# Kernel optimization log

Hardware: AMD Instinct MI355X
Metric: run time of the kernel (lower is better)

## Reference

```python
import jax, jax.numpy as jnp
import numpy as np

N, F_IN, F_OUT = 8192, 256, 128
ALPHA = 0.2  # LeakyReLU negative slope
NEG_INF = -9e15


def setup_inputs() -> dict:
    key = jax.random.key(0)
    k1, k2, k3, k4 = jax.random.split(key, 4)
    h = jax.random.normal(k1, (N, F_IN), dtype=jnp.float32)
    adj = jax.random.randint(k2, (N, N), 0, 2, dtype=jnp.int32)
    # Xavier-uniform-like init (gain=1.414)
    lim_w = 1.414 * np.sqrt(6.0 / (F_IN + F_OUT))
    W = jax.random.uniform(k3, (F_IN, F_OUT), dtype=jnp.float32, minval=-lim_w, maxval=lim_w)
    lim_a = 1.414 * np.sqrt(6.0 / (2 * F_OUT + 1))
    a = jax.random.uniform(k4, (2 * F_OUT, 1), dtype=jnp.float32, minval=-lim_a, maxval=lim_a)
    return {"h": h, "adj": adj, "W": W, "a": a}


def reference(h, adj, W, a):
    # Wh: [N, F_OUT]
    Wh = h @ W
    f_out = W.shape[1]
    # The torch code builds an [N, N, 2F] concat tensor; mathematically
    # e_ij = leakyrelu(a1 . Wh_i + a2 . Wh_j), so compute via two projections.
    a1 = a[:f_out, 0]   # [F_OUT]
    a2 = a[f_out:, 0]   # [F_OUT]
    f1 = Wh @ a1        # [N]
    f2 = Wh @ a2        # [N]
    e = jax.nn.leaky_relu(f1[:, None] + f2[None, :], negative_slope=ALPHA)  # [N, N]
    e = jnp.where(adj > 0, e, NEG_INF)
    attention = jax.nn.softmax(e, axis=1)  # [N, N]; dropout p=0 (eval mode)
    h_prime = attention @ Wh               # [N, F_OUT]
    return jax.nn.elu(h_prime)
```

## Files before the change

### kernel.cpp

```cpp
#include <hip/hip_runtime.h>
#include <hip/hip_bf16.h>
#include <math.h>

typedef short short8 __attribute__((ext_vector_type(8)));
typedef float f32x4 __attribute__((ext_vector_type(4)));
typedef int i32x4 __attribute__((ext_vector_type(4)));

#define NN 8192
#define FIN 256
#define FOUT 128
#define LRELU_A 0.2f
#define L2E 1.44269504088896f

__device__ __forceinline__ short f2bf(float x) {
    unsigned u = __builtin_bit_cast(unsigned, x);
    unsigned r = (u + 0x7FFFu + ((u >> 16) & 1u)) >> 16;
    return (short)r;
}

__global__ __launch_bounds__(256) void k_pack(const int* __restrict__ adj,
                                              unsigned* __restrict__ packed) {
    __shared__ unsigned char nib[2048];
    const int row = blockIdx.x;
    const int tid = threadIdx.x;
    const i32x4* base = (const i32x4*)(adj + (size_t)row * NN);
    #pragma unroll
    for (int q = 0; q < 8; ++q) {
        int idx = q * 256 + tid;
        i32x4 v = __builtin_nontemporal_load(base + idx);
        unsigned b = (unsigned)(v.x & 1)        | ((unsigned)(v.y & 1) << 1) |
                     ((unsigned)(v.z & 1) << 2) | ((unsigned)(v.w & 1) << 3);
        nib[idx] = (unsigned char)b;
    }
    __syncthreads();
    unsigned long long n8 = *(const unsigned long long*)&nib[tid * 8];
    unsigned w = 0;
    #pragma unroll
    for (int j = 0; j < 8; ++j)
        w |= ((unsigned)((n8 >> (8 * j)) & 0xFull)) << (4 * j);
    packed[(size_t)row * (NN / 32) + tid] = w;
}

__global__ __launch_bounds__(256) void k_wh(const float* __restrict__ h,
                                            const float* __restrict__ W,
                                            const float* __restrict__ a,
                                            float* __restrict__ Wh,
                                            float* __restrict__ f1,
                                            float* __restrict__ f2) {
    __shared__ float hs[8][FIN];
    const int tid = threadIdx.x;
    const int r0 = blockIdx.x * 8;
    #pragma unroll
    for (int i = 0; i < 2; ++i) {
        int f4 = tid + 256 * i;
        int row = f4 >> 6;
        int k4 = (f4 & 63) << 2;
        *(float4*)&hs[row][k4] = *(const float4*)(h + (size_t)(r0 + row) * FIN + k4);
    }
    __syncthreads();
    const int c4 = (tid & 31) * 4;
    const int row = tid >> 5;
    float acc0 = 0.f, acc1 = 0.f, acc2 = 0.f, acc3 = 0.f;
    #pragma unroll 4
    for (int k = 0; k < FIN; ++k) {
        float hv = hs[row][k];
        float4 w4 = *(const float4*)(W + (size_t)k * FOUT + c4);
        acc0 = fmaf(hv, w4.x, acc0);
        acc1 = fmaf(hv, w4.y, acc1);
        acc2 = fmaf(hv, w4.z, acc2);
        acc3 = fmaf(hv, w4.w, acc3);
    }
    float4 o; o.x = acc0; o.y = acc1; o.z = acc2; o.w = acc3;
    *(float4*)(Wh + (size_t)(r0 + row) * FOUT + c4) = o;

    float4 a1v = *(const float4*)(a + c4);
    float4 a2v = *(const float4*)(a + FOUT + c4);
    float p1 = acc0 * a1v.x + acc1 * a1v.y + acc2 * a1v.z + acc3 * a1v.w;
    float p2 = acc0 * a2v.x + acc1 * a2v.y + acc2 * a2v.z + acc3 * a2v.w;
    #pragma unroll
    for (int m = 1; m <= 16; m <<= 1) {
        p1 += __shfl_xor(p1, m, 64);
        p2 += __shfl_xor(p2, m, 64);
    }
    if ((tid & 31) == 0) {
        f1[r0 + row] = p1;
        f2[r0 + row] = p2;
    }
}

__global__ __launch_bounds__(256) void k_transpose(const float* __restrict__ Wh,
                                                   short* __restrict__ WhT) {
    __shared__ float t32[32][33];
    const int tid = threadIdx.x;
    const int tx = tid & 31, ty = tid >> 5;
    const int rb = (blockIdx.x & 255) * 32;
    const int cb = (blockIdx.x >> 8) * 32;
    #pragma unroll
    for (int q = 0; q < 4; ++q) {
        int r = ty + q * 8;
        t32[r][tx] = Wh[(size_t)(rb + r) * FOUT + cb + tx];
    }
    __syncthreads();
    #pragma unroll
    for (int q = 0; q < 4; ++q) {
        int c = ty + q * 8;
        WhT[(size_t)(cb + c) * NN + rb + tx] = f2bf(t32[tx][c]);
    }
}

__global__ __launch_bounds__(256) void k_gmax(const float* __restrict__ f2,
                                              float* __restrict__ gmax) {
    const int tid = threadIdx.x;
    float m = -1e30f;
    for (int i = tid; i < NN; i += 256) m = fmaxf(m, f2[i]);
    #pragma unroll
    for (int s = 1; s <= 32; s <<= 1) m = fmaxf(m, __shfl_xor(m, s, 64));
    __shared__ float red[4];
    if ((tid & 63) == 0) red[tid >> 6] = m;
    __syncthreads();
    if (tid == 0) gmax[0] = fmaxf(fmaxf(red[0], red[1]), fmaxf(red[2], red[3]));
}

__device__ __forceinline__ void gat_body(const short* __restrict__ lrd, unsigned m8,
                                         float4 fa, float4 fb,
                                         float f1r, float mh2, float& den,
                                         f32x4 acc[8]) {
    short8 b0 = *(const short8*)(lrd + 0 * 1024);
    short8 b1 = *(const short8*)(lrd + 1 * 1024);
    short8 b2 = *(const short8*)(lrd + 2 * 1024);
    short8 b3 = *(const short8*)(lrd + 3 * 1024);
    short8 b4 = *(const short8*)(lrd + 4 * 1024);
    short8 b5 = *(const short8*)(lrd + 5 * 1024);
    short8 b6 = *(const short8*)(lrd + 6 * 1024);
    short8 b7 = *(const short8*)(lrd + 7 * 1024);

    float fv[8] = {fa.x, fa.y, fa.z, fa.w, fb.x, fb.y, fb.z, fb.w};
    short8 af;
    #pragma unroll
    for (int i = 0; i < 8; ++i) {
        float e = f1r + fv[i];
        e = fmaxf(e, LRELU_A * e);
        float p = __builtin_amdgcn_exp2f(fmaf(e, L2E, -mh2));
        p = (m8 & (1u << i)) ? p : 0.0f;
        den += p;
        af[i] = f2bf(p);
    }
    acc[0] = __builtin_amdgcn_mfma_f32_16x16x32_bf16(af, b0, acc[0], 0, 0, 0);
    acc[1] = __builtin_amdgcn_mfma_f32_16x16x32_bf16(af, b1, acc[1], 0, 0, 0);
    acc[2] = __builtin_amdgcn_mfma_f32_16x16x32_bf16(af, b2, acc[2], 0, 0, 0);
    acc[3] = __builtin_amdgcn_mfma_f32_16x16x32_bf16(af, b3, acc[3], 0, 0, 0);
    acc[4] = __builtin_amdgcn_mfma_f32_16x16x32_bf16(af, b4, acc[4], 0, 0, 0);
    acc[5] = __builtin_amdgcn_mfma_f32_16x16x32_bf16(af, b5, acc[5], 0, 0, 0);
    acc[6] = __builtin_amdgcn_mfma_f32_16x16x32_bf16(af, b6, acc[6], 0, 0, 0);
    acc[7] = __builtin_amdgcn_mfma_f32_16x16x32_bf16(af, b7, acc[7], 0, 0, 0);
}

#define GAT_STEP(KOFF, MC, LRD0, LRD1, BUFW)                                       \
    {                                                                              \
        const int koff_ = (KOFF);                                                  \
        float4 fa0 = *(const float4*)(lf2 + koff_);                                \
        float4 fb0 = *(const float4*)(lf2 + koff_ + 4);                            \
        float4 fa1 = *(const float4*)(lf2 + koff_ + 32);                           \
        float4 fb1 = *(const float4*)(lf2 + koff_ + 36);                           \
        unsigned m0 = (MC.x >> mshift) & 0xffu;                                    \
        unsigned m1 = (MC.y >> mshift) & 0xffu;                                    \
        const int kpm_ = (koff_ + 128 < kchunk) ? koff_ + 128 : 0;                 \
        MC = *(const uint2*)(pkrow + (kpm_ >> 5));                                 \
        const int kst_ = (koff_ + 64 < kchunk) ? koff_ + 64 : 0;                   \
        short8 r0 = *(const short8*)(g00 + kst_);                                  \
        short8 r1 = *(const short8*)(g01 + kst_);                                  \
        short8 r2 = *(const short8*)(g10 + kst_);                                  \
        short8 r3 = *(const short8*)(g11 + kst_);                                  \
        gat_body(LRD0, m0, fa0, fb0, f1r, mh2, den, acc);                          \
        gat_body(LRD1, m1, fa1, fb1, f1r, mh2, den, acc);                          \
        *(short8*)((BUFW) + d00) = r0;                                             \
        *(short8*)((BUFW) + d01) = r1;                                             \
        *(short8*)((BUFW) + d10) = r2;                                             \
        *(short8*)((BUFW) + d11) = r3;                                             \
        asm volatile("s_waitcnt lgkmcnt(0)" ::: "memory");                         \
        __builtin_amdgcn_s_barrier();                                              \
    }

__global__ __launch_bounds__(256, 4) void k_attn(const unsigned* __restrict__ packed,
                                                 const short* __restrict__ WhT,
                                                 const float* __restrict__ f1,
                                                 const float* __restrict__ f2,
                                                 const float* __restrict__ gmax,
                                                 float* __restrict__ numb,
                                                 float* __restrict__ denb,
                                                 int kchunk, int nsplit) {
    __shared__ __align__(16) short ldsW[2][8192];
    __shared__ __align__(16) float ldsF2[2048];
    const int tid = threadIdx.x;
    const int lane = tid & 63;
    const int wave = tid >> 6;
    const int split = blockIdx.x & (nsplit - 1);
    const int rt = blockIdx.x / nsplit;
    const int rowbase = rt * 64 + wave * 16;
    const int col = lane & 15;
    const int kg = lane >> 4;
    const int arow = rowbase + col;

    const float f1r = f1[arow];
    const float gm = gmax[0];
    const float t0v = f1r + gm;
    const float mhat = fmaxf(t0v, LRELU_A * t0v);
    const float mh2 = mhat * L2E;

    const int kbase0 = split * kchunk;
    const unsigned* pkrow = packed + (size_t)arow * (NN / 32) + (kbase0 >> 5);
    const int mshift = kg * 8;
    const float* lf2 = ldsF2 + kg * 8;

    const int srow = wave * 32 + (lane >> 2);
    const int sx = srow & 7;
    const short* gsb = WhT + (size_t)srow * NN + kbase0 + (lane & 3) * 8;
    const short* g00 = gsb;
    const short* g01 = gsb + 32;
    const short* g10 = gsb + (size_t)16 * NN;
    const short* g11 = gsb + (size_t)16 * NN + 32;
    const int d00 = srow * 64        + ((((lane & 3) + 0) ^ sx) * 8);
    const int d01 = srow * 64        + ((((lane & 3) + 4) ^ sx) * 8);
    const int d10 = (srow + 16) * 64 + ((((lane & 3) + 0) ^ sx) * 8);
    const int d11 = (srow + 16) * 64 + ((((lane & 3) + 4) ^ sx) * 8);
    short* buf0 = &ldsW[0][0];
    short* buf1 = &ldsW[1][0];

    const short* lrdE0 = &ldsW[0][col * 64 + ((kg ^ (col & 7)) * 8)];
    const short* lrdE1 = &ldsW[0][col * 64 + (((kg ^ (col & 7)) * 8) ^ 32)];
    const short* lrdO0 = lrdE0 + 8192;
    const short* lrdO1 = lrdE1 + 8192;

    f32x4 acc[8] = {};
    float den = 0.0f;

    for (int i = tid * 4; i < kchunk; i += 1024)
        *(float4*)&ldsF2[i] = *(const float4*)(f2 + kbase0 + i);
    {
        short8 r0 = *(const short8*)(g00);
        short8 r1 = *(const short8*)(g01);
        short8 r2 = *(const short8*)(g10);
        short8 r3 = *(const short8*)(g11);
        *(short8*)(buf0 + d00) = r0;
        *(short8*)(buf0 + d01) = r1;
        *(short8*)(buf0 + d10) = r2;
        *(short8*)(buf0 + d11) = r3;
    }
    uint2 mA = *(const uint2*)(pkrow);
    uint2 mB = *(const uint2*)(pkrow + 2);
    asm volatile("s_waitcnt lgkmcnt(0)" ::: "memory");
    __builtin_amdgcn_s_barrier();

    for (int koff = 0; koff < kchunk; koff += 128) {
        GAT_STEP(koff,      mA, lrdE0, lrdE1, buf1);
        GAT_STEP(koff + 64, mB, lrdO0, lrdO1, buf0);
    }

    den += __shfl_xor(den, 16, 64);
    den += __shfl_xor(den, 32, 64);
    if (lane < 16) denb[(size_t)split * NN + rowbase + lane] = den;

    float* np = numb + ((size_t)split * NN + rowbase) * FOUT;
    const int rsub = (lane >> 4) * 4;
    #pragma unroll
    for (int t = 0; t < 8; ++t) {
        #pragma unroll
        for (int r = 0; r < 4; ++r) {
            np[(size_t)(rsub + r) * FOUT + t * 16 + col] = acc[t][r];
        }
    }
}

__global__ __launch_bounds__(256) void k_final(const float* __restrict__ numb,
                                               const float* __restrict__ denb,
                                               float* __restrict__ out,
                                               int splitk) {
    const int idx = blockIdx.x * 256 + threadIdx.x;
    const int row = idx >> 7;
    float s = 0.0f, d = 0.0f;
    for (int sp = 0; sp < splitk; ++sp) {
        s += numb[((size_t)sp * NN) * FOUT + idx];
        d += denb[(size_t)sp * NN + row];
    }
    float v = s / d;
    out[idx] = v > 0.0f ? v : expm1f(v);
}

extern "C" void kernel_launch(void* const* d_in, const int* in_sizes, int n_in,
                              void* d_out, int out_size, void* d_ws, size_t ws_size,
                              hipStream_t stream) {
    const float* h = (const float*)d_in[0];
    const int* adj = (const int*)d_in[1];
    const float* W = (const float*)d_in[2];
    const float* a = (const float*)d_in[3];
    float* out = (float*)d_out;

    char* ws = (char*)d_ws;
    size_t off = 0;
    auto alloc = [&](size_t nbytes) {
        char* p = ws + off;
        off = (off + nbytes + 255) & ~(size_t)255;
        return p;
    };
    float* Wh      = (float*)alloc((size_t)NN * FOUT * 4);
    short* WhT     = (short*)alloc((size_t)FOUT * NN * 2);
    float* f1      = (float*)alloc(NN * 4);
    float* f2      = (float*)alloc(NN * 4);
    float* gmx     = (float*)alloc(256);
    unsigned* pkd  = (unsigned*)alloc((size_t)NN * (NN / 32) * 4);

    int splitk = 8;
    while (splitk > 1 &&
           off + (size_t)splitk * ((size_t)NN * FOUT * 4 + NN * 4 + 512) > ws_size)
        splitk >>= 1;
    float* numb = (float*)alloc((size_t)splitk * NN * FOUT * 4);
    float* denb = (float*)alloc((size_t)splitk * NN * 4);
    const int kchunk = NN / splitk;

    k_pack<<<NN, 256, 0, stream>>>(adj, pkd);
    k_wh<<<NN / 8, 256, 0, stream>>>(h, W, a, Wh, f1, f2);
    k_transpose<<<(NN / 32) * (FOUT / 32), 256, 0, stream>>>(Wh, WhT);
    k_gmax<<<1, 256, 0, stream>>>(f2, gmx);
    k_attn<<<(NN / 64) * splitk, 256, 0, stream>>>(pkd, WhT, f1, f2, gmx, numb, denb,
                                                   kchunk, splitk);
    k_final<<<NN * FOUT / 256, 256, 0, stream>>>(numb, denb, out, splitk);
}
```

Baseline: 139.7 us.

## Fuse transpose into Wh kernel, compute softmax denominator via MFMA, simplify exp math

The Wh kernel now writes the bf16 transposed WhT directly, so the separate transpose kernel and the fp32 Wh buffer are gone. In the attention loop, the running denominator sum is replaced by an extra MFMA against a ones vector. The LeakyReLU+exp is refactored into precomputed constants and a max of two affine terms, with f2 pre-scaled by log2e. bf16 conversion now uses the library intrinsic, and launch order is adjusted. The risks are one extra MFMA per step, scattered 2-byte stores in k_wh, and a denominator summed from bf16-rounded p values.

```diff
diff --git a/kernel.cpp b/kernel.cpp
--- a/kernel.cpp
+++ b/kernel.cpp
@@ -16,6 +16,10 @@
     unsigned u = __builtin_bit_cast(unsigned, x);
     unsigned r = (u + 0x7FFFu + ((u >> 16) & 1u)) >> 16;
     return (short)r;
+}
+
+__device__ __forceinline__ short f2bf_fast(float x) {
+    return __builtin_bit_cast(short, __float2bfloat16(x));
 }
 
 __global__ __launch_bounds__(256) void k_pack(const int* __restrict__ adj,
@@ -44,7 +48,7 @@
 __global__ __launch_bounds__(256) void k_wh(const float* __restrict__ h,
                                             const float* __restrict__ W,
                                             const float* __restrict__ a,
-                                            float* __restrict__ Wh,
+                                            short* __restrict__ WhT,
                                             float* __restrict__ f1,
                                             float* __restrict__ f2) {
     __shared__ float hs[8][FIN];
@@ -70,8 +74,11 @@
         acc2 = fmaf(hv, w4.z, acc2);
         acc3 = fmaf(hv, w4.w, acc3);
     }
-    float4 o; o.x = acc0; o.y = acc1; o.z = acc2; o.w = acc3;
-    *(float4*)(Wh + (size_t)(r0 + row) * FOUT + c4) = o;
+    const int wr = r0 + row;
+    WhT[(size_t)(c4 + 0) * NN + wr] = f2bf(acc0);
+    WhT[(size_t)(c4 + 1) * NN + wr] = f2bf(acc1);
+    WhT[(size_t)(c4 + 2) * NN + wr] = f2bf(acc2);
+    WhT[(size_t)(c4 + 3) * NN + wr] = f2bf(acc3);
 
     float4 a1v = *(const float4*)(a + c4);
     float4 a2v = *(const float4*)(a + FOUT + c4);
@@ -83,28 +90,8 @@
         p2 += __shfl_xor(p2, m, 64);
     }
     if ((tid & 31) == 0) {
-        f1[r0 + row] = p1;
-        f2[r0 + row] = p2;
-    }
-}
-
-__global__ __launch_bounds__(256) void k_transpose(const float* __restrict__ Wh,
-                                                   short* __restrict__ WhT) {
-    __shared__ float t32[32][33];
-    const int tid = threadIdx.x;
-    const int tx = tid & 31, ty = tid >> 5;
-    const int rb = (blockIdx.x & 255) * 32;
-    const int cb = (blockIdx.x >> 8) * 32;
-    #pragma unroll
-    for (int q = 0; q < 4; ++q) {
-        int r = ty + q * 8;
-        t32[r][tx] = Wh[(size_t)(rb + r) * FOUT + cb + tx];
-    }
-    __syncthreads();
-    #pragma unroll
-    for (int q = 0; q < 4; ++q) {
-        int c = ty + q * 8;
-        WhT[(size_t)(cb + c) * NN + rb + tx] = f2bf(t32[tx][c]);
+        f1[wr] = p1;
+        f2[wr] = p2;
     }
 }
 
@@ -123,8 +110,8 @@
 
 __device__ __forceinline__ void gat_body(const short* __restrict__ lrd, unsigned m8,
                                          float4 fa, float4 fb,
-                                         float f1r, float mh2, float& den,
-                                         f32x4 acc[8]) {
+                                         float c1, float c2,
+                                         f32x4 acc[9], short8 ones) {
     short8 b0 = *(const short8*)(lrd + 0 * 1024);
     short8 b1 = *(const short8*)(lrd + 1 * 1024);
     short8 b2 = *(const short8*)(lrd + 2 * 1024);
@@ -138,12 +125,11 @@
     short8 af;
     #pragma unroll
     for (int i = 0; i < 8; ++i) {
-        float e = f1r + fv[i];
-        e = fmaxf(e, LRELU_A * e);
-        float p = __builtin_amdgcn_exp2f(fmaf(e, L2E, -mh2));
+        float u = fv[i] + c1;
+        float v = fmaf(LRELU_A, fv[i], c2);
+        float p = __builtin_amdgcn_exp2f(fmaxf(u, v));
         p = (m8 & (1u << i)) ? p : 0.0f;
-        den += p;
-        af[i] = f2bf(p);
+        af[i] = f2bf_fast(p);
     }
     acc[0] = __builtin_amdgcn_mfma_f32_16x16x32_bf16(af, b0, acc[0], 0, 0, 0);
     acc[1] = __builtin_amdgcn_mfma_f32_16x16x32_bf16(af, b1, acc[1], 0, 0, 0);
@@ -153,6 +139,7 @@
     acc[5] = __builtin_amdgcn_mfma_f32_16x16x32_bf16(af, b5, acc[5], 0, 0, 0);
     acc[6] = __builtin_amdgcn_mfma_f32_16x16x32_bf16(af, b6, acc[6], 0, 0, 0);
     acc[7] = __builtin_amdgcn_mfma_f32_16x16x32_bf16(af, b7, acc[7], 0, 0, 0);
+    acc[8] = __builtin_amdgcn_mfma_f32_16x16x32_bf16(af, ones, acc[8], 0, 0, 0);
 }
 
 #define GAT_STEP(KOFF, MC, LRD0, LRD1, BUFW)                                       \
@@ -171,8 +158,8 @@
         short8 r1 = *(const short8*)(g01 + kst_);                                  \
         short8 r2 = *(const short8*)(g10 + kst_);                                  \
         short8 r3 = *(const short8*)(g11 + kst_);                                  \
-        gat_body(LRD0, m0, fa0, fb0, f1r, mh2, den, acc);                          \
-        gat_body(LRD1, m1, fa1, fb1, f1r, mh2, den, acc);                          \
+        gat_body(LRD0, m0, fa0, fb0, c1, c2, acc, ones);                           \
+        gat_body(LRD1, m1, fa1, fb1, c1, c2, acc, ones);                           \
         *(short8*)((BUFW) + d00) = r0;                                             \
         *(short8*)((BUFW) + d01) = r1;                                             \
         *(short8*)((BUFW) + d10) = r2;                                             \
@@ -206,6 +193,11 @@
     const float t0v = f1r + gm;
     const float mhat = fmaxf(t0v, LRELU_A * t0v);
     const float mh2 = mhat * L2E;
+    const float c1 = fmaf(f1r, L2E, -mh2);
+    const float c2 = fmaf(LRELU_A * f1r, L2E, -mh2);
+
+    const short8 ones = {0x3F80, 0x3F80, 0x3F80, 0x3F80,
+                         0x3F80, 0x3F80, 0x3F80, 0x3F80};
 
     const int kbase0 = split * kchunk;
     const unsigned* pkrow = packed + (size_t)arow * (NN / 32) + (kbase0 >> 5);
@@ -231,11 +223,13 @@
     const short* lrdO0 = lrdE0 + 8192;
     const short* lrdO1 = lrdE1 + 8192;
 
-    f32x4 acc[8] = {};
-    float den = 0.0f;
-
-    for (int i = tid * 4; i < kchunk; i += 1024)
-        *(float4*)&ldsF2[i] = *(const float4*)(f2 + kbase0 + i);
+    f32x4 acc[9] = {};
+
+    for (int i = tid * 4; i < kchunk; i += 1024) {
+        float4 v = *(const float4*)(f2 + kbase0 + i);
+        v.x *= L2E; v.y *= L2E; v.z *= L2E; v.w *= L2E;
+        *(float4*)&ldsF2[i] = v;
+    }
     {
         short8 r0 = *(const short8*)(g00);
         short8 r1 = *(const short8*)(g01);
@@ -256,12 +250,14 @@
         GAT_STEP(koff + 64, mB, lrdO0, lrdO1, buf0);
     }
 
-    den += __shfl_xor(den, 16, 64);
-    den += __shfl_xor(den, 32, 64);
-    if (lane < 16) denb[(size_t)split * NN + rowbase + lane] = den;
+    const int rsub = (lane >> 4) * 4;
+    if (col == 0) {
+        #pragma unroll
+        for (int r = 0; r < 4; ++r)
+            denb[(size_t)split * NN + rowbase + rsub + r] = acc[8][r];
+    }
 
     float* np = numb + ((size_t)split * NN + rowbase) * FOUT;
-    const int rsub = (lane >> 4) * 4;
     #pragma unroll
     for (int t = 0; t < 8; ++t) {
         #pragma unroll
@@ -302,7 +298,6 @@
         off = (off + nbytes + 255) & ~(size_t)255;
         return p;
     };
-    float* Wh      = (float*)alloc((size_t)NN * FOUT * 4);
     short* WhT     = (short*)alloc((size_t)FOUT * NN * 2);
     float* f1      = (float*)alloc(NN * 4);
     float* f2      = (float*)alloc(NN * 4);
@@ -317,10 +312,9 @@
     float* denb = (float*)alloc((size_t)splitk * NN * 4);
     const int kchunk = NN / splitk;
 
+    k_wh<<<NN / 8, 256, 0, stream>>>(h, W, a, WhT, f1, f2);
+    k_gmax<<<1, 256, 0, stream>>>(f2, gmx);
     k_pack<<<NN, 256, 0, stream>>>(adj, pkd);
-    k_wh<<<NN / 8, 256, 0, stream>>>(h, W, a, Wh, f1, f2);
-    k_transpose<<<(NN / 32) * (FOUT / 32), 256, 0, stream>>>(Wh, WhT);
-    k_gmax<<<1, 256, 0, stream>>>(f2, gmx);
     k_attn<<<(NN / 64) * splitk, 256, 0, stream>>>(pkd, WhT, f1, f2, gmx, numb, denb,
                                                    kchunk, splitk);
     k_final<<<NN * FOUT / 256, 256, 0, stream>>>(numb, denb, out, splitk);
```

Result: faster. 132.8 us (-4.9%).
